# Kernel optimization log

Hardware: AMD Instinct MI355X
Metric: run time of the kernel (lower is better)

## Reference

```python
import jax, jax.numpy as jnp
import numpy as np

NUM_ROI = 200

def mish(x):
    return x * jnp.tanh(jax.nn.softplus(x))

def gcn_conv(x, edge_index, edge_weight, W, b):
    # PyG GCNConv: add self-loops (weight 1), symmetric normalization, aggregate at target (col)
    N = x.shape[0]
    row, col = edge_index[0], edge_index[1]
    loop = jnp.arange(N)
    row = jnp.concatenate([row, loop])
    col = jnp.concatenate([col, loop])
    w = jnp.concatenate([edge_weight, jnp.ones((N,), x.dtype)])
    deg = jax.ops.segment_sum(w, col, num_segments=N)
    dis = jnp.where(deg > 0, jax.lax.rsqrt(deg), 0.0)
    norm = dis[row] * w * dis[col]                       # [E+N]
    h = x @ W                                            # [N, out]
    out = jax.ops.segment_sum(h[row] * norm[:, None], col, num_segments=N)
    return out + b

def setup_inputs() -> dict:
    key = jax.random.key(0)
    ks = jax.random.split(key, 16)
    B, E = 256, 1638400
    N = B * NUM_ROI
    d = {}
    d['x'] = jax.random.normal(ks[0], (N, NUM_ROI), jnp.float32)
    d['edge_index'] = jax.random.randint(ks[1], (2, E), 0, N, jnp.int64)
    d['edge_attr'] = jax.random.uniform(ks[2], (E,), jnp.float32)
    def rn(k, shape, fan_in):
        return jax.random.normal(k, shape, jnp.float32) * (1.0 / np.sqrt(fan_in))
    d['W1'] = rn(ks[3], (NUM_ROI, 128), NUM_ROI); d['b1'] = jnp.zeros((128,), jnp.float32)
    d['W2'] = rn(ks[4], (128, 64), 128);          d['b2'] = jnp.zeros((64,), jnp.float32)
    d['Wro'] = rn(ks[5], (64, 8), 64);            d['bro'] = jnp.zeros((8,), jnp.float32)
    d['Wfc1'] = rn(ks[6], (8 * NUM_ROI, NUM_ROI), 8 * NUM_ROI); d['bfc1'] = jnp.zeros((NUM_ROI,), jnp.float32)
    d['bn_gamma'] = jnp.ones((NUM_ROI,), jnp.float32)
    d['bn_beta'] = jnp.zeros((NUM_ROI,), jnp.float32)
    d['Wfc2'] = rn(ks[7], (NUM_ROI, 2), NUM_ROI); d['bfc2'] = jnp.zeros((2,), jnp.float32)
    d['Wd1'] = rn(ks[8], (NUM_ROI, 64), NUM_ROI); d['bd1'] = jnp.zeros((64,), jnp.float32)
    d['Wd2'] = rn(ks[9], (64, 6), 64);            d['bd2'] = jnp.zeros((6,), jnp.float32)
    return d

def reference(x, edge_index, edge_attr, W1, b1, W2, b2, Wro, bro, Wfc1, bfc1,
              bn_gamma, bn_beta, Wfc2, bfc2, Wd1, bd1, Wd2, bd2):
    h = mish(gcn_conv(x, edge_index, edge_attr, W1, b1))
    h = mish(gcn_conv(h, edge_index, edge_attr, W2, b2))
    out = mish(h @ Wro + bro)                            # [N, 8]
    feat = out.reshape(-1, NUM_ROI * 8)                  # [B, 1600]
    z = feat @ Wfc1 + bfc1                               # [B, numROI]
    # BatchNorm1d in training mode (batch statistics, biased variance)
    mu = jnp.mean(z, axis=0)
    var = jnp.mean((z - mu) ** 2, axis=0)
    zn = (z - mu) * jax.lax.rsqrt(var + 1e-5) * bn_gamma + bn_beta
    mid = mish(zn)
    logits = mid @ Wfc2 + bfc2                           # [B, 2]
    rev = 2.0 * jax.lax.stop_gradient(mid) - mid
    cls_logits = jax.nn.relu(rev @ Wd1 + bd1) @ Wd2 + bd2  # [B, 6]
    return (logits, cls_logits)
```

## Files before the change

### kernel.cpp

```cpp
#include <hip/hip_runtime.h>
#include <hip/hip_bf16.h>

typedef __hip_bfloat16 bf16;
typedef __attribute__((ext_vector_type(8))) short short8;
typedef __attribute__((ext_vector_type(4))) float f32x4;

#define NROI 200
#define EPB 6400
#define SPB 6400

__device__ __forceinline__ float u2f(unsigned short u) {
  return __uint_as_float(((unsigned)u) << 16);
}
__device__ __forceinline__ float lo16(unsigned u) { return __uint_as_float(u << 16); }
__device__ __forceinline__ float hi16(unsigned u) { return __uint_as_float(u & 0xffff0000u); }
__device__ __forceinline__ float b2f(bf16 v) { return __bfloat162float(v); }
__device__ __forceinline__ unsigned short f2us(float f) {
  union { bf16 b; unsigned short u; } c;
  c.b = __float2bfloat16(f);
  return c.u;
}

__device__ __forceinline__ float mishf(float x) {
  float sp = (x > 20.0f) ? x : log1pf(expf(x));
  return x * tanhf(sp);
}

__global__ __launch_bounds__(256) void detect_kernel(const unsigned short* xu,
                                                     const unsigned* eiw,
                                                     int* flags) {
  int tid = threadIdx.x;
  int sane = 0, zodd = 0;
  for (int i = tid; i < 4096; i += 256) {
    unsigned short u = xu[2 * i];
    unsigned e = (u >> 7) & 0xFF;
    if (u == 0 || (e >= 100 && e <= 134)) sane++;
  }
  for (int i = tid; i < 4096; i += 256) {
    if (eiw[2 * i + 1] == 0) zodd++;
  }
  __shared__ int s1[256], s2[256];
  s1[tid] = sane; s2[tid] = zodd;
  __syncthreads();
  for (int off = 128; off > 0; off >>= 1) {
    if (tid < off) { s1[tid] += s1[tid + off]; s2[tid] += s2[tid + off]; }
    __syncthreads();
  }
  if (tid == 0) {
    flags[0] = (s1[0] < 2048) ? 1 : 0;
    flags[1] = (s2[0] > 2048) ? 1 : 0;
  }
}

struct WArgs {
  const void* src[16];
  int n[16];
  int off[16];
};

__global__ __launch_bounds__(256) void convert_weights(WArgs a, bf16* base,
                                                       unsigned short* __restrict__ w1swz,
                                                       unsigned short* __restrict__ w2swz,
                                                       const int* flags) {
  int t = blockIdx.y;
  int i = blockIdx.x * 256 + threadIdx.x;
  int isf32 = flags[0];
  if (t < 16) {
    if (i >= a.n[t]) return;
    bf16* dst = base + a.off[t];
    if (isf32) dst[i] = __float2bfloat16(((const float*)a.src[t])[i]);
    else ((unsigned short*)dst)[i] = ((const unsigned short*)a.src[t])[i];
    return;
  }
  int w1 = (t == 16);
  int K  = w1 ? 200 : 128;
  int NT = w1 ? 8 : 4;
  int KC = w1 ? 7 : 4;
  int total = KC * NT * 512;
  if (i >= total) return;
  int e = i & 7;
  int l = (i >> 3) & 63;
  int tt = (i >> 9) % NT;
  int kc = i / (NT * 512);
  int k = kc * 32 + (l >> 4) * 8 + e;
  int c = tt * 16 + (l & 15);
  unsigned short v = 0;
  if (k < K) {
    const void* src = w1 ? a.src[0] : a.src[2];
    if (isf32) v = f2us(((const float*)src)[k * (NT * 16) + c]);
    else v = ((const unsigned short*)src)[k * (NT * 16) + c];
  }
  (w1 ? w1swz : w2swz)[i] = v;
}


__global__ __launch_bounds__(1024, 1) void count_lds(const int* __restrict__ ei,
                                                     const void* __restrict__ ea,
                                                     const int* __restrict__ flags,
                                                     unsigned* __restrict__ cnt8g,
                                                     unsigned* __restrict__ ws16g,
                                                     unsigned char* __restrict__ rank8,
                                                     int NU, int NW, int E) {
  extern __shared__ unsigned smem[];
  unsigned* s_cnt = smem;
  unsigned* s_ws  = smem + NU;
  int tid = threadIdx.x;
  int blk = blockIdx.x;
  for (int i = tid; i < NU + NW; i += 1024) smem[i] = 0;
  __syncthreads();
  int is64 = flags[1], isf32 = flags[0];
  long long base = (long long)blk * EPB;
  for (int k = 0; k < EPB; k += 1024) {
    int ko = k + tid;
    long long e = base + ko;
    if (ko < EPB && e < E) {
      int c = is64 ? __builtin_nontemporal_load(&ei[2 * ((long long)E + e)])
                   : __builtin_nontemporal_load(&ei[(long long)E + e]);
      float w = isf32 ? __builtin_nontemporal_load(&((const float*)ea)[e])
                      : u2f(__builtin_nontemporal_load(&((const unsigned short*)ea)[e]));
      w = fminf(fmaxf(w, 0.0f), 15.0f);
      unsigned sh = (unsigned)(c & 3) * 8;
      unsigned old = atomicAdd(&s_cnt[c >> 2], 1u << sh);
      rank8[e] = (unsigned char)((old >> sh) & 0xFF);
      unsigned wi = __float2uint_rn(w * 4096.0f);
      atomicAdd(&s_ws[c >> 1], (c & 1) ? (wi << 16) : wi);
    }
  }
  __syncthreads();
  for (int i = tid; i < NU; i += 1024)
    __builtin_nontemporal_store(s_cnt[i], &cnt8g[(size_t)blk * NU + i]);
  for (int i = tid; i < NW; i += 1024)
    __builtin_nontemporal_store(s_ws[i], &ws16g[(size_t)blk * NW + i]);
}

__global__ __launch_bounds__(256) void reduce_r1(unsigned* __restrict__ cnt8g,
                                                 const unsigned* __restrict__ ws16g,
                                                 unsigned* __restrict__ cntpart,
                                                 unsigned* __restrict__ wspart,
                                                 int NU, int NW, int nblk, int bpg) {
  int col = blockIdx.x * 256 + threadIdx.x;
  int gy = blockIdx.y;
  if (col >= NU) return;
  unsigned run = 0;
  unsigned r0 = 0, r1 = 0, r2 = 0, r3 = 0;
  int b0 = gy * bpg;
  int be = b0 + bpg; if (be > nblk) be = nblk;
  for (int b = b0; b < be; ++b) {
    unsigned v = cnt8g[(size_t)b * NU + col];
    cnt8g[(size_t)b * NU + col] = run;
    run += v;
    unsigned wA = ws16g[(size_t)b * NW + 2 * col];
    unsigned wB = ws16g[(size_t)b * NW + 2 * col + 1];
    r0 += wA & 0xFFFF; r1 += wA >> 16;
    r2 += wB & 0xFFFF; r3 += wB >> 16;
  }
  cntpart[(size_t)gy * NU + col] = run;
  unsigned* wp = &wspart[((size_t)gy * NU + col) * 4];
  wp[0] = r0; wp[1] = r1; wp[2] = r2; wp[3] = r3;
}

__global__ __launch_bounds__(256) void combine_k(const unsigned* __restrict__ cntpart,
                                                 const unsigned* __restrict__ wspart,
                                                 unsigned* __restrict__ gybase,
                                                 int* __restrict__ cnt,
                                                 float* __restrict__ dis,
                                                 int* __restrict__ bsum,
                                                 int NU, int N) {
  __shared__ int ts[256];
  int col = blockIdx.x * 256 + threadIdx.x;
  int mysum = 0;
  if (col < NU) {
    unsigned g = 0;
#pragma unroll
    for (int gy = 0; gy < 4; ++gy) {
      unsigned t = cntpart[(size_t)gy * NU + col];
      gybase[(size_t)gy * NU + col] = g;
      g += t;
    }
    unsigned ws[4] = {0, 0, 0, 0};
#pragma unroll
    for (int gy = 0; gy < 4; ++gy) {
      const unsigned* wp = &wspart[((size_t)gy * NU + col) * 4];
#pragma unroll
      for (int j = 0; j < 4; ++j) ws[j] += wp[j];
    }
#pragma unroll
    for (int j = 0; j < 4; ++j) {
      int n = 4 * col + j;
      if (n < N) {
        int cj = (int)((g >> (8 * j)) & 0xFF);
        cnt[n] = cj;
        mysum += cj;
        dis[n] = rsqrtf(1.0f + (float)ws[j] * 0.000244140625f);
      }
    }
  }
  int tid = threadIdx.x;
  ts[tid] = mysum;
  __syncthreads();
  for (int off = 128; off > 0; off >>= 1) {
    if (tid < off) ts[tid] += ts[tid + off];
    __syncthreads();
  }
  if (tid == 0) bsum[blockIdx.x] = ts[0];
}

__global__ __launch_bounds__(256) void scan_phase3(const int* __restrict__ cnt,
                                                   const int* __restrict__ bsum,
                                                   int* __restrict__ ptr,
                                                   int nb, int N) {
  __shared__ int ts[256];
  int blk = blockIdx.x;
  int tid = threadIdx.x;
  int bpre = 0;
  for (int i = 0; i < blk; ++i) bpre += bsum[i];
  int base = blk * 1024 + tid * 4;
  int c0 = 0, c1 = 0, c2 = 0, c3 = 0;
  if (base + 0 < N) c0 = cnt[base + 0];
  if (base + 1 < N) c1 = cnt[base + 1];
  if (base + 2 < N) c2 = cnt[base + 2];
  if (base + 3 < N) c3 = cnt[base + 3];
  ts[tid] = c0 + c1 + c2 + c3;
  __syncthreads();
  for (int off = 1; off < 256; off <<= 1) {
    int v = ts[tid];
    if (tid >= off) v += ts[tid - off];
    __syncthreads();
    ts[tid] = v;
    __syncthreads();
  }
  int run = bpre + (tid ? ts[tid - 1] : 0);
  if (base + 0 < N) { ptr[base + 0] = run; run += c0; }
  if (base + 1 < N) { ptr[base + 1] = run; run += c1; }
  if (base + 2 < N) { ptr[base + 2] = run; run += c2; }
  if (base + 3 < N) { ptr[base + 3] = run; run += c3; }
  if (blk == nb - 1 && tid == 255) ptr[N] = bpre + ts[255];
}

__global__ __launch_bounds__(1024, 1) void scatter_lds(const int* __restrict__ ei,
                                                       const void* __restrict__ ea,
                                                       const int* __restrict__ flags,
                                                       const float* __restrict__ dis,
                                                       const int* __restrict__ ptr,
                                                       const unsigned* __restrict__ cnt8g,
                                                       const unsigned* __restrict__ gybase,
                                                       const unsigned char* __restrict__ rank8,
                                                       long long* __restrict__ epair,
                                                       int NU, int bpg, int E) {
  extern __shared__ unsigned smem[];
  unsigned* s_pb = smem;
  unsigned* s_gb = smem + NU;
  int tid = threadIdx.x;
  int blk = blockIdx.x;
  int gy = blk / bpg;
  for (int i = tid; i < NU; i += 1024) s_pb[i] = cnt8g[(size_t)blk * NU + i];
  for (int i = tid; i < NU; i += 1024) s_gb[i] = gybase[(size_t)gy * NU + i];
  __syncthreads();
  int is64 = flags[1], isf32 = flags[0];
  long long base = (long long)blk * SPB;
  for (int k = 0; k < SPB; k += 1024) {
    int ko = k + tid;
    long long e = base + ko;
    if (ko < SPB && e < E) {
      int r = is64 ? __builtin_nontemporal_load(&ei[2 * e])
                   : __builtin_nontemporal_load(&ei[e]);
      int c = is64 ? __builtin_nontemporal_load(&ei[2 * ((long long)E + e)])
                   : __builtin_nontemporal_load(&ei[(long long)E + e]);
      float w = isf32 ? __builtin_nontemporal_load(&((const float*)ea)[e])
                      : u2f(__builtin_nontemporal_load(&((const unsigned short*)ea)[e]));
      float nrm = dis[r] * w * dis[c];
      unsigned sh = (unsigned)(c & 3) * 8;
      unsigned p1 = (s_pb[c >> 2] >> sh) & 0xFF;
      unsigned p2 = (s_gb[c >> 2] >> sh) & 0xFF;
      int idx = ptr[c] + (int)p1 + (int)p2 + (int)rank8[e];
      long long pr = (long long)((unsigned long long)__float_as_uint(nrm) << 32) |
                     (unsigned)r;
      __builtin_nontemporal_store(pr, &epair[idx]);
    }
  }
}

template<int KC, int NT, int DYN>
__global__ __launch_bounds__(256) void gemm_mfma(const void* __restrict__ A,
                                                 int Ktrue,
                                                 const int* __restrict__ flags,
                                                 const unsigned short* __restrict__ Wswz,
                                                 unsigned short* __restrict__ H,
                                                 int M) {
  int wid = threadIdx.x >> 6, lane = threadIdx.x & 63;
  int row0 = (blockIdx.x * 4 + wid) * 16;
  if (row0 >= M) return;
  constexpr int NC = NT * 16;
  int isf32 = DYN ? flags[0] : 0;
  f32x4 acc[NT];
#pragma unroll
  for (int t = 0; t < NT; ++t) acc[t] = {0.f, 0.f, 0.f, 0.f};
  int arow = row0 + (lane & 15);
  int kbase = (lane >> 4) * 8;
  const float* Af = (const float*)A;
  const unsigned short* Au = (const unsigned short*)A;
#pragma unroll
  for (int kc = 0; kc < KC; ++kc) {
    int k0 = kbase + kc * 32;
    short8 a = {0, 0, 0, 0, 0, 0, 0, 0};
    if (k0 + 8 <= Ktrue) {
      size_t off = (size_t)arow * Ktrue + k0;
      if (DYN && isf32) {
        f32x4 f0 = __builtin_nontemporal_load((const f32x4*)&Af[off]);
        f32x4 f1 = __builtin_nontemporal_load((const f32x4*)&Af[off + 4]);
        a[0] = (short)f2us(f0[0]); a[1] = (short)f2us(f0[1]);
        a[2] = (short)f2us(f0[2]); a[3] = (short)f2us(f0[3]);
        a[4] = (short)f2us(f1[0]); a[5] = (short)f2us(f1[1]);
        a[6] = (short)f2us(f1[2]); a[7] = (short)f2us(f1[3]);
      } else {
        a = *(const short8*)&Au[off];
      }
    }
#pragma unroll
    for (int t = 0; t < NT; ++t) {
      short8 b = *(const short8*)&Wswz[((kc * NT + t) * 64 + lane) * 8];
      acc[t] = __builtin_amdgcn_mfma_f32_16x16x32_bf16(a, b, acc[t], 0, 0, 0);
    }
  }
  int orow = row0 + (lane >> 4) * 4;
  int ocol = lane & 15;
#pragma unroll
  for (int t = 0; t < NT; ++t)
#pragma unroll
    for (int r = 0; r < 4; ++r)
      H[(size_t)(orow + r) * NC + t * 16 + ocol] = f2us(acc[t][r]);
}

__global__ __launch_bounds__(256) void agg_mish128(const unsigned* __restrict__ hu,
                                                   const float* __restrict__ dis,
                                                   const int* __restrict__ ptr,
                                                   const long long* __restrict__ ep,
                                                   const bf16* __restrict__ bias,
                                                   unsigned* __restrict__ g, int N) {
  int w = threadIdx.x >> 6, lane = threadIdx.x & 63;
  int n = blockIdx.x * 4 + w;
  float dn = dis[n];
  float self = dn * dn;
  unsigned u = hu[((unsigned)n << 6) + lane];
  float acc0 = lo16(u) * self;
  float acc1 = hi16(u) * self;
  int e0 = ptr[n], e1 = ptr[n + 1];
  for (int base = e0; base < e1; base += 64) {
    long long myp = 0;
    if (base + lane < e1) myp = __builtin_nontemporal_load(&ep[base + lane]);
    int mx = (int)(unsigned)myp;
    int my = (int)(myp >> 32);
    int m = e1 - base; if (m > 64) m = 64;
    int j = 0;
    for (; j + 8 <= m; j += 8) {
      unsigned uu[8]; float ww[8];
#pragma unroll
      for (int q = 0; q < 8; ++q) {
        unsigned rr = (unsigned)__builtin_amdgcn_readlane(mx, j + q);
        uu[q] = hu[(rr << 6) + lane];
        ww[q] = __uint_as_float(__builtin_amdgcn_readlane(my, j + q));
      }
#pragma unroll
      for (int q = 0; q < 8; ++q) {
        acc0 += lo16(uu[q]) * ww[q];
        acc1 += hi16(uu[q]) * ww[q];
      }
    }
    for (; j < m; ++j) {
      unsigned rr = (unsigned)__builtin_amdgcn_readlane(mx, j);
      float ww = __uint_as_float(__builtin_amdgcn_readlane(my, j));
      unsigned uu = hu[(rr << 6) + lane];
      acc0 += lo16(uu) * ww;
      acc1 += hi16(uu) * ww;
    }
  }
  unsigned bb = ((const unsigned*)bias)[lane];
  float m0 = mishf(acc0 + lo16(bb));
  float m1 = mishf(acc1 + hi16(bb));
  __builtin_nontemporal_store(((unsigned)f2us(m1) << 16) | f2us(m0),
                              &g[((unsigned)n << 6) + lane]);
}

__global__ __launch_bounds__(256) void agg_mish64_ro(const unsigned short* __restrict__ hus,
                                                     const float* __restrict__ dis,
                                                     const int* __restrict__ ptr,
                                                     const long long* __restrict__ ep,
                                                     const bf16* __restrict__ bias,
                                                     const bf16* __restrict__ Wro,
                                                     const bf16* __restrict__ bro,
                                                     float* __restrict__ out8, int N) {
  int w = threadIdx.x >> 6, lane = threadIdx.x & 63;
  int n = blockIdx.x * 4 + w;
  float dn = dis[n];
  float self = dn * dn;
  float acc = u2f(hus[((unsigned)n << 6) + lane]) * self;
  int e0 = ptr[n], e1 = ptr[n + 1];
  for (int base = e0; base < e1; base += 64) {
    long long myp = 0;
    if (base + lane < e1) myp = __builtin_nontemporal_load(&ep[base + lane]);
    int mx = (int)(unsigned)myp;
    int my = (int)(myp >> 32);
    int m = e1 - base; if (m > 64) m = 64;
    int j = 0;
    for (; j + 8 <= m; j += 8) {
      float vv[8], ww[8];
#pragma unroll
      for (int q = 0; q < 8; ++q) {
        unsigned rr = (unsigned)__builtin_amdgcn_readlane(mx, j + q);
        vv[q] = u2f(hus[(rr << 6) + lane]);
        ww[q] = __uint_as_float(__builtin_amdgcn_readlane(my, j + q));
      }
#pragma unroll
      for (int q = 0; q < 8; ++q) acc += vv[q] * ww[q];
    }
    for (; j < m; ++j) {
      unsigned rr = (unsigned)__builtin_amdgcn_readlane(mx, j);
      float ww = __uint_as_float(__builtin_amdgcn_readlane(my, j));
      acc += u2f(hus[(rr << 6) + lane]) * ww;
    }
  }
  float mv = mishf(acc + u2f(((const unsigned short*)bias)[lane]));
  uint4 wr = ((const uint4*)Wro)[lane];
  float p0 = mv * lo16(wr.x), p1 = mv * hi16(wr.x);
  float p2 = mv * lo16(wr.y), p3 = mv * hi16(wr.y);
  float p4 = mv * lo16(wr.z), p5 = mv * hi16(wr.z);
  float p6 = mv * lo16(wr.w), p7 = mv * hi16(wr.w);
  bool b0 = lane & 1;
  float q0 = (b0 ? p4 : p0) + __shfl_xor(b0 ? p0 : p4, 1);
  float q1 = (b0 ? p5 : p1) + __shfl_xor(b0 ? p1 : p5, 1);
  float q2 = (b0 ? p6 : p2) + __shfl_xor(b0 ? p2 : p6, 1);
  float q3 = (b0 ? p7 : p3) + __shfl_xor(b0 ? p3 : p7, 1);
  bool b1 = lane & 2;
  float r0 = (b1 ? q2 : q0) + __shfl_xor(b1 ? q0 : q2, 2);
  float r1 = (b1 ? q3 : q1) + __shfl_xor(b1 ? q1 : q3, 2);
  bool b2v = lane & 4;
  float t = (b2v ? r1 : r0) + __shfl_xor(b2v ? r0 : r1, 4);
  t += __shfl_xor(t, 8);
  t += __shfl_xor(t, 16);
  t += __shfl_xor(t, 32);
  if (lane < 8) {
    int oidx = ((lane & 1) << 2) | (lane & 2) | ((lane >> 2) & 1);
    out8[(size_t)n * 8 + oidx] = mishf(t + u2f(((const unsigned short*)bro)[oidx]));
  }
}


__global__ __launch_bounds__(256) void fc1_kernel(const float* __restrict__ feat,
                                                  const bf16* __restrict__ W,
                                                  const bf16* __restrict__ bias,
                                                  float* __restrict__ z) {
  __shared__ float fr[1600];
  int b = blockIdx.x, tid = threadIdx.x;
  for (int i = tid; i < 1600; i += 256) fr[i] = feat[(size_t)b * 1600 + i];
  __syncthreads();
  if (tid < NROI) {
    float acc = b2f(bias[tid]);
#pragma unroll 8
    for (int k = 0; k < 1600; ++k) acc += fr[k] * b2f(W[k * NROI + tid]);
    z[b * NROI + tid] = acc;
  }
}

__global__ __launch_bounds__(256) void bn_stats(const float* __restrict__ z,
                                                float* mu, float* rvar, int B) {
  int j = blockIdx.x;
  int tid = threadIdx.x;
  float v = z[tid * NROI + j];
  float s = v, q = v * v;
  for (int off = 32; off > 0; off >>= 1) {
    s += __shfl_down(s, off);
    q += __shfl_down(q, off);
  }
  __shared__ float ss[4], qq[4];
  int w = tid >> 6, lane = tid & 63;
  if (lane == 0) { ss[w] = s; qq[w] = q; }
  __syncthreads();
  if (tid == 0) {
    float S = ss[0] + ss[1] + ss[2] + ss[3];
    float Q = qq[0] + qq[1] + qq[2] + qq[3];
    float m = S / (float)B;
    float var = Q / (float)B - m * m;
    mu[j] = m;
    rvar[j] = rsqrtf(var + 1e-5f);
  }
}

__global__ __launch_bounds__(256) void head_kernel(const float* __restrict__ z,
                                                   const float* __restrict__ mu,
                                                   const float* __restrict__ rvar,
                                                   const bf16* __restrict__ gamma,
                                                   const bf16* __restrict__ beta,
                                                   const bf16* __restrict__ Wfc2,
                                                   const bf16* __restrict__ bfc2,
                                                   const bf16* __restrict__ Wd1,
                                                   const bf16* __restrict__ bd1,
                                                   const bf16* __restrict__ Wd2,
                                                   const bf16* __restrict__ bd2,
                                                   float* __restrict__ out, int B) {
  __shared__ float mid[NROI];
  __shared__ float t[64];
  int b = blockIdx.x, tid = threadIdx.x;
  if (tid < NROI) {
    float v = (z[b * NROI + tid] - mu[tid]) * rvar[tid] * b2f(gamma[tid]) + b2f(beta[tid]);
    mid[tid] = mishf(v);
  }
  __syncthreads();
  if (tid < 64) {
    float acc = b2f(bd1[tid]);
#pragma unroll 8
    for (int j = 0; j < NROI; ++j) acc += mid[j] * b2f(Wd1[j * 64 + tid]);
    t[tid] = fmaxf(acc, 0.0f);
  }
  if (tid >= 64 && tid < 66) {
    int c = tid - 64;
    float acc = b2f(bfc2[c]);
    for (int j = 0; j < NROI; ++j) acc += mid[j] * b2f(Wfc2[j * 2 + c]);
    out[b * 2 + c] = acc;
  }
  __syncthreads();
  if (tid < 6) {
    float acc = b2f(bd2[tid]);
#pragma unroll 8
    for (int k = 0; k < 64; ++k) acc += t[k] * b2f(Wd2[k * 6 + tid]);
    out[B * 2 + b * 6 + tid] = acc;
  }
}


extern "C" void kernel_launch(void* const* d_in, const int* in_sizes, int n_in,
                              void* d_out, int out_size, void* d_ws, size_t ws_size,
                              hipStream_t stream) {
  const void* x  = d_in[0];
  const int*  ei = (const int*)d_in[1];
  const void* ea = d_in[2];
  float* out = (float*)d_out;

  int N = in_sizes[0] / NROI;
  int E = in_sizes[2];
  int B = N / NROI;

  int NU = (N + 3) / 4;
  int NW = (N + 1) / 2;
  int nblk = (E + EPB - 1) / EPB;
  int bpg = (nblk + 3) / 4;
  int nsb = (E + SPB - 1) / SPB;

  char* p = (char*)d_ws;
  auto carve = [&](size_t bytes) -> void* {
    void* r = (void*)p;
    p += (bytes + 255) & ~(size_t)255;
    return r;
  };
  int*   flags = (int*)carve(16);
  bf16*  cw    = (bf16*)carve(400000 * 2);
  float* dis   = (float*)carve((size_t)N * 4);
  unsigned* cnt8g  = (unsigned*)carve((size_t)nblk * NU * 4);
  unsigned* ws16g  = (unsigned*)carve((size_t)nblk * NW * 4);
  unsigned* cntpart = (unsigned*)carve((size_t)4 * NU * 4);
  unsigned* wspart  = (unsigned*)carve((size_t)4 * NU * 16);
  unsigned* gybase  = (unsigned*)carve((size_t)4 * NU * 4);
  unsigned char* rank8 = (unsigned char*)carve((size_t)E);
  int*   cnt   = (int*)carve((size_t)N * 4);
  int*   ptr   = (int*)carve(((size_t)N + 1) * 4);
  int*   bsum  = (int*)carve(1024);
  long long* epair = (long long*)carve((size_t)E * 8);
  unsigned short* h = (unsigned short*)carve((size_t)N * 128 * 2);
  unsigned* g = (unsigned*)carve((size_t)N * 128 * 2);
  unsigned short* w1swz = (unsigned short*)carve(7 * 8 * 512 * 2);
  unsigned short* w2swz = (unsigned short*)carve(4 * 4 * 512 * 2);
  float* out8  = (float*)carve((size_t)N * 8 * 4);
  float* z     = (float*)carve((size_t)B * NROI * 4);
  float* mu    = (float*)carve(NROI * 4);
  float* rv    = (float*)carve(NROI * 4);

  WArgs wa;
  int run = 0;
  int maxn = 0;
  for (int t = 0; t < 16; ++t) {
    wa.src[t] = d_in[3 + t];
    wa.n[t]   = in_sizes[3 + t];
    wa.off[t] = run;
    run += in_sizes[3 + t];
    if (in_sizes[3 + t] > maxn) maxn = in_sizes[3 + t];
  }
  const bf16* W1   = cw + wa.off[0];
  const bf16* b1   = cw + wa.off[1];
  const bf16* W2   = cw + wa.off[2];
  const bf16* b2   = cw + wa.off[3];
  const bf16* Wro  = cw + wa.off[4];
  const bf16* bro  = cw + wa.off[5];
  const bf16* Wfc1 = cw + wa.off[6];
  const bf16* bfc1 = cw + wa.off[7];
  const bf16* gam  = cw + wa.off[8];
  const bf16* bet  = cw + wa.off[9];
  const bf16* Wfc2 = cw + wa.off[10];
  const bf16* bfc2 = cw + wa.off[11];
  const bf16* Wd1  = cw + wa.off[12];
  const bf16* bd1  = cw + wa.off[13];
  const bf16* Wd2  = cw + wa.off[14];
  const bf16* bd2  = cw + wa.off[15];

  detect_kernel<<<1, 256, 0, stream>>>((const unsigned short*)x,
                                       (const unsigned*)ei, flags);
  dim3 wg((maxn + 255) / 256, 18);
  convert_weights<<<wg, 256, 0, stream>>>(wa, cw, w1swz, w2swz, flags);

  size_t cntLds = (size_t)(NU + NW) * 4;
  count_lds<<<nblk, 1024, cntLds, stream>>>(ei, ea, flags, cnt8g, ws16g,
                                            rank8, NU, NW, E);
  dim3 rg((NU + 255) / 256, 4);
  reduce_r1<<<rg, 256, 0, stream>>>(cnt8g, ws16g, cntpart, wspart,
                                    NU, NW, nblk, bpg);
  int ncomb = (NU + 255) / 256;
  combine_k<<<ncomb, 256, 0, stream>>>(cntpart, wspart, gybase, cnt, dis,
                                       bsum, NU, N);
  scan_phase3<<<ncomb, 256, 0, stream>>>(cnt, bsum, ptr, ncomb, N);

  size_t scLds = (size_t)2 * NU * 4;
  scatter_lds<<<nsb, 1024, scLds, stream>>>(ei, ea, flags, dis, ptr, cnt8g,
                                            gybase, rank8, epair, NU, bpg, E);

  gemm_mfma<7, 8, 1><<<N / 64, 256, 0, stream>>>(x, 200, flags, w1swz, h, N);
  agg_mish128<<<N / 4, 256, 0, stream>>>((const unsigned*)h, dis, ptr, epair,
                                         b1, g, N);
  gemm_mfma<4, 4, 0><<<N / 64, 256, 0, stream>>>(g, 128, flags, w2swz, h, N);
  agg_mish64_ro<<<N / 4, 256, 0, stream>>>(h, dis, ptr, epair, b2, Wro, bro,
                                           out8, N);

  fc1_kernel<<<B, 256, 0, stream>>>(out8, Wfc1, bfc1, z);
  bn_stats<<<NROI, 256, 0, stream>>>(z, mu, rv, B);
  head_kernel<<<B, 256, 0, stream>>>(z, mu, rv, gam, bet, Wfc2, bfc2,
                                     Wd1, bd1, Wd2, bd2, out, B);
}
```

Measured before the change: 376.0 us.

## Pack edge source and bf16 weight into 32 bits, factor out target normalization

Each CSR edge entry shrinks from a 64-bit (fp32 norm, row) pair to a 32-bit word: the 16-bit source index in the upper half and a bf16 of dis[row]*w in the lower half. The dis[col] factor is removed from every edge and applied once per node after aggregation, which also turns the self-loop term into h*dis. The aim is to halve the edge-list traffic in the scatter and in both aggregation passes. The counting granularity (EPB) is doubled, and scatter blocks now index count tables by blk>>1. The cost is bf16 rounding of edge weights, and the packing only works while N stays below 65536.

```diff
diff --git a/kernel.cpp b/kernel.cpp
--- a/kernel.cpp
+++ b/kernel.cpp
@@ -6,7 +6,7 @@
 typedef __attribute__((ext_vector_type(4))) float f32x4;
 
 #define NROI 200
-#define EPB 6400
+#define EPB 12800
 #define SPB 6400
 
 __device__ __forceinline__ float u2f(unsigned short u) {
@@ -245,15 +245,16 @@
                                                        const unsigned* __restrict__ cnt8g,
                                                        const unsigned* __restrict__ gybase,
                                                        const unsigned char* __restrict__ rank8,
-                                                       long long* __restrict__ epair,
+                                                       unsigned* __restrict__ epair,
                                                        int NU, int bpg, int E) {
   extern __shared__ unsigned smem[];
   unsigned* s_pb = smem;
   unsigned* s_gb = smem + NU;
   int tid = threadIdx.x;
   int blk = blockIdx.x;
-  int gy = blk / bpg;
-  for (int i = tid; i < NU; i += 1024) s_pb[i] = cnt8g[(size_t)blk * NU + i];
+  int cblk = blk >> 1;
+  int gy = cblk / bpg;
+  for (int i = tid; i < NU; i += 1024) s_pb[i] = cnt8g[(size_t)cblk * NU + i];
   for (int i = tid; i < NU; i += 1024) s_gb[i] = gybase[(size_t)gy * NU + i];
   __syncthreads();
   int is64 = flags[1], isf32 = flags[0];
@@ -268,13 +269,12 @@
                    : __builtin_nontemporal_load(&ei[(long long)E + e]);
       float w = isf32 ? __builtin_nontemporal_load(&((const float*)ea)[e])
                       : u2f(__builtin_nontemporal_load(&((const unsigned short*)ea)[e]));
-      float nrm = dis[r] * w * dis[c];
+      float disw = dis[r] * w;
       unsigned sh = (unsigned)(c & 3) * 8;
       unsigned p1 = (s_pb[c >> 2] >> sh) & 0xFF;
       unsigned p2 = (s_gb[c >> 2] >> sh) & 0xFF;
       int idx = ptr[c] + (int)p1 + (int)p2 + (int)rank8[e];
-      long long pr = (long long)((unsigned long long)__float_as_uint(nrm) << 32) |
-                     (unsigned)r;
+      unsigned pr = ((unsigned)r << 16) | f2us(disw);
       __builtin_nontemporal_store(pr, &epair[idx]);
     }
   }
@@ -334,31 +334,28 @@
 __global__ __launch_bounds__(256) void agg_mish128(const unsigned* __restrict__ hu,
                                                    const float* __restrict__ dis,
                                                    const int* __restrict__ ptr,
-                                                   const long long* __restrict__ ep,
+                                                   const unsigned* __restrict__ ep,
                                                    const bf16* __restrict__ bias,
                                                    unsigned* __restrict__ g, int N) {
   int w = threadIdx.x >> 6, lane = threadIdx.x & 63;
   int n = blockIdx.x * 4 + w;
   float dn = dis[n];
-  float self = dn * dn;
   unsigned u = hu[((unsigned)n << 6) + lane];
-  float acc0 = lo16(u) * self;
-  float acc1 = hi16(u) * self;
+  float acc0 = lo16(u) * dn;
+  float acc1 = hi16(u) * dn;
   int e0 = ptr[n], e1 = ptr[n + 1];
   for (int base = e0; base < e1; base += 64) {
-    long long myp = 0;
+    unsigned myp = 0;
     if (base + lane < e1) myp = __builtin_nontemporal_load(&ep[base + lane]);
-    int mx = (int)(unsigned)myp;
-    int my = (int)(myp >> 32);
     int m = e1 - base; if (m > 64) m = 64;
     int j = 0;
     for (; j + 8 <= m; j += 8) {
       unsigned uu[8]; float ww[8];
 #pragma unroll
       for (int q = 0; q < 8; ++q) {
-        unsigned rr = (unsigned)__builtin_amdgcn_readlane(mx, j + q);
-        uu[q] = hu[(rr << 6) + lane];
-        ww[q] = __uint_as_float(__builtin_amdgcn_readlane(my, j + q));
+        unsigned pk = (unsigned)__builtin_amdgcn_readlane((int)myp, j + q);
+        uu[q] = hu[((pk >> 16) << 6) + lane];
+        ww[q] = u2f((unsigned short)pk);
       }
 #pragma unroll
       for (int q = 0; q < 8; ++q) {
@@ -367,16 +364,16 @@
       }
     }
     for (; j < m; ++j) {
-      unsigned rr = (unsigned)__builtin_amdgcn_readlane(mx, j);
-      float ww = __uint_as_float(__builtin_amdgcn_readlane(my, j));
-      unsigned uu = hu[(rr << 6) + lane];
+      unsigned pk = (unsigned)__builtin_amdgcn_readlane((int)myp, j);
+      unsigned uu = hu[((pk >> 16) << 6) + lane];
+      float ww = u2f((unsigned short)pk);
       acc0 += lo16(uu) * ww;
       acc1 += hi16(uu) * ww;
     }
   }
   unsigned bb = ((const unsigned*)bias)[lane];
-  float m0 = mishf(acc0 + lo16(bb));
-  float m1 = mishf(acc1 + hi16(bb));
+  float m0 = mishf(acc0 * dn + lo16(bb));
+  float m1 = mishf(acc1 * dn + hi16(bb));
   __builtin_nontemporal_store(((unsigned)f2us(m1) << 16) | f2us(m0),
                               &g[((unsigned)n << 6) + lane]);
 }
@@ -384,7 +381,7 @@
 __global__ __launch_bounds__(256) void agg_mish64_ro(const unsigned short* __restrict__ hus,
                                                      const float* __restrict__ dis,
                                                      const int* __restrict__ ptr,
-                                                     const long long* __restrict__ ep,
+                                                     const unsigned* __restrict__ ep,
                                                      const bf16* __restrict__ bias,
                                                      const bf16* __restrict__ Wro,
                                                      const bf16* __restrict__ bro,
@@ -392,34 +389,30 @@
   int w = threadIdx.x >> 6, lane = threadIdx.x & 63;
   int n = blockIdx.x * 4 + w;
   float dn = dis[n];
-  float self = dn * dn;
-  float acc = u2f(hus[((unsigned)n << 6) + lane]) * self;
+  float acc = u2f(hus[((unsigned)n << 6) + lane]) * dn;
   int e0 = ptr[n], e1 = ptr[n + 1];
   for (int base = e0; base < e1; base += 64) {
-    long long myp = 0;
+    unsigned myp = 0;
     if (base + lane < e1) myp = __builtin_nontemporal_load(&ep[base + lane]);
-    int mx = (int)(unsigned)myp;
-    int my = (int)(myp >> 32);
     int m = e1 - base; if (m > 64) m = 64;
     int j = 0;
     for (; j + 8 <= m; j += 8) {
       float vv[8], ww[8];
 #pragma unroll
       for (int q = 0; q < 8; ++q) {
-        unsigned rr = (unsigned)__builtin_amdgcn_readlane(mx, j + q);
-        vv[q] = u2f(hus[(rr << 6) + lane]);
-        ww[q] = __uint_as_float(__builtin_amdgcn_readlane(my, j + q));
+        unsigned pk = (unsigned)__builtin_amdgcn_readlane((int)myp, j + q);
+        vv[q] = u2f(hus[((pk >> 16) << 6) + lane]);
+        ww[q] = u2f((unsigned short)pk);
       }
 #pragma unroll
       for (int q = 0; q < 8; ++q) acc += vv[q] * ww[q];
     }
     for (; j < m; ++j) {
-      unsigned rr = (unsigned)__builtin_amdgcn_readlane(mx, j);
-      float ww = __uint_as_float(__builtin_amdgcn_readlane(my, j));
-      acc += u2f(hus[(rr << 6) + lane]) * ww;
-    }
-  }
-  float mv = mishf(acc + u2f(((const unsigned short*)bias)[lane]));
+      unsigned pk = (unsigned)__builtin_amdgcn_readlane((int)myp, j);
+      acc += u2f(hus[((pk >> 16) << 6) + lane]) * u2f((unsigned short)pk);
+    }
+  }
+  float mv = mishf(acc * dn + u2f(((const unsigned short*)bias)[lane]));
   uint4 wr = ((const uint4*)Wro)[lane];
   float p0 = mv * lo16(wr.x), p1 = mv * hi16(wr.x);
   float p2 = mv * lo16(wr.y), p3 = mv * hi16(wr.y);
@@ -563,7 +556,7 @@
   int*   cnt   = (int*)carve((size_t)N * 4);
   int*   ptr   = (int*)carve(((size_t)N + 1) * 4);
   int*   bsum  = (int*)carve(1024);
-  long long* epair = (long long*)carve((size_t)E * 8);
+  unsigned* epair = (unsigned*)carve((size_t)E * 4);
   unsigned short* h = (unsigned short*)carve((size_t)N * 128 * 2);
   unsigned* g = (unsigned*)carve((size_t)N * 128 * 2);
   unsigned short* w1swz = (unsigned short*)carve(7 * 8 * 512 * 2);
```

New measurement: 348.5 us. 1.08x faster.
